# Optimization experiments

Hardware: AMD Instinct MI355X
Metric: run time of the kernel (lower is better)

The kernel has to match this reference:

```python
import jax, jax.numpy as jnp
import numpy as np

N = 20000
E = 320000
IN_C = 256
HID = 64
OUT_C = 64
NUM_LAYERS = 3
HEADS = 8


def setup_inputs() -> dict:
    key = jax.random.key(0)
    ks = jax.random.split(key, 12)
    s_in = 1.0 / np.sqrt(IN_C)
    s_h = 1.0 / np.sqrt(HID)
    inp = {
        "x": jax.random.normal(ks[0], (N, IN_C), dtype=jnp.float32),
        "edge_index": jax.random.randint(ks[1], (2, E), 0, N, dtype=jnp.int64),
        "lin1_w": jax.random.uniform(ks[2], (IN_C, HID), jnp.float32, -s_in, s_in),
        "lin1_b": jnp.zeros((HID,), jnp.float32),
        "wq": jax.random.uniform(ks[3], (NUM_LAYERS, HID, HID), jnp.float32, -s_h, s_h),
        "bq": jnp.zeros((NUM_LAYERS, HID), jnp.float32),
        "wk": jax.random.uniform(ks[4], (NUM_LAYERS, HID, HID), jnp.float32, -s_h, s_h),
        "bk": jnp.zeros((NUM_LAYERS, HID), jnp.float32),
        "wv": jax.random.uniform(ks[5], (NUM_LAYERS, HID, HID), jnp.float32, -s_h, s_h),
        "bv": jnp.zeros((NUM_LAYERS, HID), jnp.float32),
        "lin2_w": jax.random.uniform(ks[6], (HID, OUT_C), jnp.float32, -s_h, s_h),
        "lin2_b": jnp.zeros((OUT_C,), jnp.float32),
    }
    return inp


def reference(x, edge_index, lin1_w, lin1_b, wq, bq, wk, bk, wv, bv, lin2_w, lin2_b):
    n = x.shape[0]
    C = lin1_w.shape[1]
    d = C // HEADS  # per-head dim
    inv_sqrt_d = 1.0 / (d ** 0.5)

    # gcn_norm with self-loops (symmetric normalization, edge weights = 1)
    loop = jnp.arange(n, dtype=edge_index.dtype)
    row = jnp.concatenate([edge_index[0], loop])  # source j
    col = jnp.concatenate([edge_index[1], loop])  # target i
    deg = jax.ops.segment_sum(jnp.ones_like(col, dtype=x.dtype), col, num_segments=n)
    dinv = jnp.where(deg > 0, deg ** -0.5, 0.0)
    norm = dinv[row] * dinv[col]  # [E+N]

    # input projection (dropout inactive in eval mode)
    h = jax.nn.relu(x @ lin1_w + lin1_b)
    x_all = h[:, None, :]  # [N, 1, C] growing history

    for l in range(NUM_LAYERS):
        t = x_all.shape[1]
        # node-level projections (linear commutes with gather)
        q = x_all[:, -1] @ wq[l] + bq[l]                      # [N, C]
        k = jnp.einsum("ntc,cd->ntd", x_all, wk[l]) + bk[l]   # [N, t, C]
        v = jnp.einsum("ntc,cd->ntd", x_all, wv[l]) + bv[l]   # [N, t, C]
        # per-edge multi-head attention of target's latest repr over source history
        Qe = q[col].reshape(-1, HEADS, d)                      # [E', H, d]
        Ke = k[row].reshape(-1, t, HEADS, d)                   # [E', t, H, d]
        Ve = v[row].reshape(-1, t, HEADS, d)
        scores = jnp.einsum("ehd,ethd->eht", Qe, Ke) * inv_sqrt_d
        attn = jax.nn.softmax(scores, axis=-1)                 # [E', H, t]
        msg = jnp.einsum("eht,ethd->ehd", attn, Ve).reshape(-1, C)
        msg = msg * norm[:, None]
        out = jax.ops.segment_sum(msg, col, num_segments=n)    # sum aggregation
        out = jax.nn.relu(out)
        x_all = jnp.concatenate([x_all, out[:, None, :]], axis=1)

    logits = x_all[:, -1] @ lin2_w + lin2_b
    return jax.nn.log_softmax(logits, axis=1)
```

## Files before the change

### kernel.cpp

```cpp
#include <hip/hip_runtime.h>
#include <math.h>

#define HID 64
#define HEADS 8
#define NUM_LAYERS 3

typedef __attribute__((ext_vector_type(8))) short bf16x8;
typedef __attribute__((ext_vector_type(4))) float f32x4;

__device__ __forceinline__ unsigned short f2bf(float f) {
    union { float f; unsigned int u; } cv; cv.f = f;
    unsigned int u = cv.u;
    unsigned int r = (u + 0x7FFFu + ((u >> 16) & 1u)) >> 16;
    return (unsigned short)r;
}
__device__ __forceinline__ float bflo(unsigned int u) {
    union { unsigned int u; float f; } cv; cv.u = u << 16; return cv.f;
}
__device__ __forceinline__ float bfhi(unsigned int u) {
    union { unsigned int u; float f; } cv; cv.u = u & 0xFFFF0000u; return cv.f;
}
__device__ __forceinline__ unsigned relu_pk(unsigned u) {
    unsigned m = ((u & 0x8000u) ? 0u : 0xFFFFu) |
                 ((u & 0x80000000u) ? 0u : 0xFFFF0000u);
    return u & m;
}

__global__ void k_count(const int* __restrict__ col, int* __restrict__ counts, int E) {
    int e = blockIdx.x * blockDim.x + threadIdx.x;
    if (e < E) atomicAdd(&counts[col[e]], 1);
}

__global__ __launch_bounds__(1024) void k_scan(const int* __restrict__ counts,
                                               int* __restrict__ start,
                                               float* __restrict__ dinv, int n) {
    __shared__ int wsum[16];
    int tid = threadIdx.x;
    int lane = tid & 63, wv = tid >> 6;
    int ipt = (n + 1023) >> 10;
    int c0 = tid * ipt;
    int c1 = min(n, c0 + ipt);
    int s = 0;
    for (int i = c0; i < c1; ++i) s += counts[i];
    int x = s;
#pragma unroll
    for (int off = 1; off < 64; off <<= 1) {
        int y = __shfl_up(x, off);
        if (lane >= off) x += y;
    }
    if (lane == 63) wsum[wv] = x;
    __syncthreads();
    if (wv == 0 && lane < 16) {
        int t2 = wsum[lane];
#pragma unroll
        for (int off = 1; off < 16; off <<= 1) {
            int y = __shfl_up(t2, off);
            if (lane >= off) t2 += y;
        }
        wsum[lane] = t2;
    }
    __syncthreads();
    int waveoff = (wv > 0) ? wsum[wv - 1] : 0;
    int run = waveoff + x - s;
    for (int i = c0; i < c1; ++i) {
        int v = counts[i];
        start[i] = run;
        dinv[i] = rsqrtf((float)(v + 1));
        run += v;
    }
    if (tid == 0) start[n] = wsum[15];
}

__global__ void k_scatter(const int* __restrict__ ei, const int* __restrict__ start,
                          int* __restrict__ fill, int* __restrict__ ebuf, int E) {
    int e = blockIdx.x * blockDim.x + threadIdx.x;
    if (e >= E) return;
    int r = ei[e], c = ei[E + e];
    int pos = start[c] + atomicAdd(&fill[c], 1);
    ebuf[pos] = r;
}

#define ALD 72

__device__ __forceinline__ void stage_w_bf16(unsigned short* Wt,
                                             const float* __restrict__ w, int tid) {
    for (int idx = tid; idx < 1024; idx += 256) {
        int k = idx >> 4, n4 = (idx & 15) * 4;
        float4 wv = *(const float4*)&w[k * 64 + n4];
        Wt[(n4 + 0) * ALD + k] = f2bf(wv.x);
        Wt[(n4 + 1) * ALD + k] = f2bf(wv.y);
        Wt[(n4 + 2) * ALD + k] = f2bf(wv.z);
        Wt[(n4 + 3) * ALD + k] = f2bf(wv.w);
    }
}

__device__ __forceinline__ void mfma_step(const unsigned short* Alds,
                                          const unsigned short* Wt,
                                          int tid, f32x4 acc[4]) {
    int lane = tid & 63;
    int m0 = (tid >> 6) * 16;
    int c16 = lane & 15, quad = lane >> 4;
    const unsigned short* ar = &Alds[(m0 + c16) * ALD + quad * 8];
    bf16x8 a0 = *(const bf16x8*)ar;
    bf16x8 a1 = *(const bf16x8*)(ar + 32);
#pragma unroll
    for (int nt = 0; nt < 4; ++nt) {
        const unsigned short* br = &Wt[(nt * 16 + c16) * ALD + quad * 8];
        bf16x8 b0 = *(const bf16x8*)br;
        bf16x8 b1 = *(const bf16x8*)(br + 32);
        acc[nt] = __builtin_amdgcn_mfma_f32_16x16x32_bf16(a0, b0, acc[nt], 0, 0, 0);
        acc[nt] = __builtin_amdgcn_mfma_f32_16x16x32_bf16(a1, b1, acc[nt], 0, 0, 0);
    }
}

__global__ __launch_bounds__(256, 4) void k_lin1(
    const float* __restrict__ x, const float* __restrict__ w,
    const float* __restrict__ b, const float* __restrict__ wv0,
    const float* __restrict__ bv0, unsigned short* __restrict__ h,
    unsigned short* __restrict__ kv, int n) {
    __shared__ __align__(16) unsigned short Alds[64 * ALD];
    __shared__ __align__(16) unsigned short Wt[64 * ALD];
    int tid = threadIdx.x;
    int node0 = blockIdx.x * 64;
    f32x4 acc[4];
#pragma unroll
    for (int nt = 0; nt < 4; ++nt) acc[nt] = (f32x4){0.f, 0.f, 0.f, 0.f};

    for (int kc = 0; kc < 256; kc += 64) {
        __syncthreads();
        stage_w_bf16(Wt, w + kc * 64, tid);
        for (int idx = tid; idx < 1024; idx += 256) {
            int r = idx >> 4, c4 = (idx & 15) * 4;
            int node = node0 + r;
            float4 v = make_float4(0.f, 0.f, 0.f, 0.f);
            if (node < n) v = *(const float4*)&x[(size_t)node * 256 + kc + c4];
            Alds[r * ALD + c4 + 0] = f2bf(v.x);
            Alds[r * ALD + c4 + 1] = f2bf(v.y);
            Alds[r * ALD + c4 + 2] = f2bf(v.z);
            Alds[r * ALD + c4 + 3] = f2bf(v.w);
        }
        __syncthreads();
        mfma_step(Alds, Wt, tid, acc);
    }
    int lane = tid & 63;
    int m0 = (tid >> 6) * 16, c16 = lane & 15, quad = lane >> 4;
    float bias[4];
#pragma unroll
    for (int nt = 0; nt < 4; ++nt) bias[nt] = b[nt * 16 + c16];

    __syncthreads();
    stage_w_bf16(Wt, wv0, tid);
#pragma unroll
    for (int i = 0; i < 4; ++i) {
        int row = m0 + quad * 4 + i;
        int node = node0 + row;
#pragma unroll
        for (int nt = 0; nt < 4; ++nt) {
            unsigned short hb = f2bf(fmaxf(acc[nt][i] + bias[nt], 0.f));
            Alds[row * ALD + nt * 16 + c16] = hb;
            if (node < n) h[(size_t)node * 64 + nt * 16 + c16] = hb;
        }
    }
    __syncthreads();
    f32x4 acc2[4];
#pragma unroll
    for (int nt = 0; nt < 4; ++nt) acc2[nt] = (f32x4){0.f, 0.f, 0.f, 0.f};
    mfma_step(Alds, Wt, tid, acc2);
    float bias2[4];
#pragma unroll
    for (int nt = 0; nt < 4; ++nt) bias2[nt] = bv0[nt * 16 + c16];
#pragma unroll
    for (int i = 0; i < 4; ++i) {
        int node = node0 + m0 + quad * 4 + i;
        if (node < n) {
#pragma unroll
            for (int nt = 0; nt < 4; ++nt)
                kv[(size_t)node * 64 + nt * 16 + c16] = f2bf(acc2[nt][i] + bias2[nt]);
        }
    }
}

__global__ __launch_bounds__(256, 4) void k_qkv(
    const unsigned short* __restrict__ xsbase,
    const float* __restrict__ wq, const float* __restrict__ bq,
    const float* __restrict__ wk, const float* __restrict__ bk,
    const float* __restrict__ wv, const float* __restrict__ bv,
    float* __restrict__ q, unsigned short* __restrict__ kv,
    int n, int layer, int t, int kv_stride) {
    int job = blockIdx.y;
    const unsigned short* src; const float* w; const float* b; bool relu_in;
    int kv_off = 0;
    if (job == 0) {
        src = xsbase + (size_t)layer * n * 64;
        w = wq + layer * 4096; b = bq + layer * 64;
        relu_in = (layer >= 1);
    } else if (job <= t) {
        int s = job - 1;
        src = xsbase + (size_t)s * n * 64;
        w = wk + layer * 4096; b = bk + layer * 64;
        kv_off = s * 128;
        relu_in = (s >= 1);
    } else {
        int s = job - t - 1;
        src = xsbase + (size_t)s * n * 64;
        w = wv + layer * 4096; b = bv + layer * 64;
        kv_off = s * 128 + 64;
        relu_in = (s >= 1);
    }
    __shared__ __align__(16) unsigned short Alds[64 * ALD];
    __shared__ __align__(16) unsigned short Wt[64 * ALD];
    int tid = threadIdx.x;
    int node0 = blockIdx.x * 64;
    stage_w_bf16(Wt, w, tid);
    for (int idx = tid; idx < 512; idx += 256) {
        int r = idx >> 3, seg = idx & 7;
        int node = node0 + r;
        uint4 u = make_uint4(0u, 0u, 0u, 0u);
        if (node < n) u = *(const uint4*)&src[(size_t)node * 64 + seg * 8];
        if (relu_in) {
            u.x = relu_pk(u.x); u.y = relu_pk(u.y);
            u.z = relu_pk(u.z); u.w = relu_pk(u.w);
        }
        *(uint4*)&Alds[r * ALD + seg * 8] = u;
    }
    __syncthreads();
    f32x4 acc[4];
#pragma unroll
    for (int nt = 0; nt < 4; ++nt) acc[nt] = (f32x4){0.f, 0.f, 0.f, 0.f};
    mfma_step(Alds, Wt, tid, acc);

    int lane = tid & 63;
    int m0 = (tid >> 6) * 16, c16 = lane & 15, quad = lane >> 4;
    float bias[4];
#pragma unroll
    for (int nt = 0; nt < 4; ++nt) bias[nt] = b[nt * 16 + c16];
    if (job == 0) {
#pragma unroll
        for (int i = 0; i < 4; ++i) {
            int node = node0 + m0 + quad * 4 + i;
            if (node < n) {
#pragma unroll
                for (int nt = 0; nt < 4; ++nt)
                    q[(size_t)node * 64 + nt * 16 + c16] = acc[nt][i] + bias[nt];
            }
        }
    } else {
#pragma unroll
        for (int i = 0; i < 4; ++i) {
            int node = node0 + m0 + quad * 4 + i;
            if (node < n) {
#pragma unroll
                for (int nt = 0; nt < 4; ++nt)
                    kv[(size_t)node * kv_stride + kv_off + nt * 16 + c16] =
                        f2bf(acc[nt][i] + bias[nt]);
            }
        }
    }
}

template <int T>
__global__ __launch_bounds__(256) void k_attn_g(
    const int* __restrict__ start, const int* __restrict__ ebuf,
    const float* __restrict__ dinv, const float* __restrict__ q,
    const unsigned short* __restrict__ kv, unsigned short* __restrict__ outp, int n) {
    const int KVS = (T == 1) ? 64 : T * 128;
    int node = (int)((blockIdx.x * (size_t)blockDim.x + threadIdx.x) >> 6);
    int lane = threadIdx.x & 63;
    if (node >= n) return;
    int g = lane >> 3;
    int cb = (lane & 7) * 8;
    const float isd = 0.35355339059327373f;

    float qv[8];
    if (T > 1) {
        float4 q0 = *(const float4*)&q[(size_t)node * 64 + cb];
        float4 q1 = *(const float4*)&q[(size_t)node * 64 + cb + 4];
        qv[0] = q0.x; qv[1] = q0.y; qv[2] = q0.z; qv[3] = q0.w;
        qv[4] = q1.x; qv[5] = q1.y; qv[6] = q1.z; qv[7] = q1.w;
    }
    float dc = dinv[node];
    int s0 = start[node];
    int cnt = start[node + 1] - s0 + 1;

    float acc[8];
#pragma unroll
    for (int k = 0; k < 8; ++k) acc[k] = 0.f;

    for (int base = 0; base < cnt; base += 8) {
        int idx = base + g;
        bool valid = idx < cnt;
        int r = node;
        if (valid && idx > 0) r = ebuf[s0 + idx - 1];
        float dr = valid ? dinv[r] : 0.f;
        const unsigned short* rkv = kv + (size_t)r * KVS;

        float sc[T];
        float wgt;
        if (T > 1) {
            float m = -1e30f;
#pragma unroll
            for (int s = 0; s < T; ++s) {
                uint4 ku = *(const uint4*)&rkv[s * 128 + cb];
                float p = qv[0] * bflo(ku.x) + qv[1] * bfhi(ku.x)
                        + qv[2] * bflo(ku.y) + qv[3] * bfhi(ku.y)
                        + qv[4] * bflo(ku.z) + qv[5] * bfhi(ku.z)
                        + qv[6] * bflo(ku.w) + qv[7] * bfhi(ku.w);
                p *= isd;
                sc[s] = p;
                m = fmaxf(m, p);
            }
            float denom = 0.f;
#pragma unroll
            for (int s = 0; s < T; ++s) { sc[s] = __expf(sc[s] - m); denom += sc[s]; }
            wgt = dr / denom;
        } else {
            sc[0] = 1.f;
            wgt = dr;
        }

        float mg[8];
#pragma unroll
        for (int k = 0; k < 8; ++k) mg[k] = 0.f;
#pragma unroll
        for (int s = 0; s < T; ++s) {
            uint4 vu = *(const uint4*)&rkv[((T == 1) ? 0 : s * 128 + 64) + cb];
            float wv_ = sc[s];
            mg[0] += wv_ * bflo(vu.x); mg[1] += wv_ * bfhi(vu.x);
            mg[2] += wv_ * bflo(vu.y); mg[3] += wv_ * bfhi(vu.y);
            mg[4] += wv_ * bflo(vu.z); mg[5] += wv_ * bfhi(vu.z);
            mg[6] += wv_ * bflo(vu.w); mg[7] += wv_ * bfhi(vu.w);
        }
#pragma unroll
        for (int k = 0; k < 8; ++k) acc[k] += wgt * mg[k];
    }

#pragma unroll
    for (int off = 8; off < 64; off <<= 1) {
#pragma unroll
        for (int k = 0; k < 8; ++k) acc[k] += __shfl_xor(acc[k], off);
    }
    if (g == 0) {
        ushort4 o0, o1;
        o0.x = f2bf(acc[0] * dc); o0.y = f2bf(acc[1] * dc);
        o0.z = f2bf(acc[2] * dc); o0.w = f2bf(acc[3] * dc);
        o1.x = f2bf(acc[4] * dc); o1.y = f2bf(acc[5] * dc);
        o1.z = f2bf(acc[6] * dc); o1.w = f2bf(acc[7] * dc);
        *(ushort4*)&outp[(size_t)node * 64 + cb] = o0;
        *(ushort4*)&outp[(size_t)node * 64 + cb + 4] = o1;
    }
}

__global__ __launch_bounds__(256) void k_attn3f(
    const int* __restrict__ start, const int* __restrict__ ebuf,
    const float* __restrict__ dinv, const float* __restrict__ q,
    const unsigned short* __restrict__ kv,
    const float* __restrict__ w2, const float* __restrict__ b2,
    float* __restrict__ outp, int n) {
    const int T = 3, KVS = 384;
    int node = (int)((blockIdx.x * (size_t)blockDim.x + threadIdx.x) >> 6);
    int lane = threadIdx.x & 63;
    if (node >= n) return;
    int g = lane >> 3;
    int cb = (lane & 7) * 8;
    const float isd = 0.35355339059327373f;

    float qv[8];
    {
        float4 q0 = *(const float4*)&q[(size_t)node * 64 + cb];
        float4 q1 = *(const float4*)&q[(size_t)node * 64 + cb + 4];
        qv[0] = q0.x; qv[1] = q0.y; qv[2] = q0.z; qv[3] = q0.w;
        qv[4] = q1.x; qv[5] = q1.y; qv[6] = q1.z; qv[7] = q1.w;
    }
    float dc = dinv[node];
    int s0 = start[node];
    int cnt = start[node + 1] - s0 + 1;

    float acc[8];
#pragma unroll
    for (int k = 0; k < 8; ++k) acc[k] = 0.f;

    for (int base = 0; base < cnt; base += 8) {
        int idx = base + g;
        bool valid = idx < cnt;
        int r = node;
        if (valid && idx > 0) r = ebuf[s0 + idx - 1];
        float dr = valid ? dinv[r] : 0.f;
        const unsigned short* rkv = kv + (size_t)r * KVS;

        float sc[T];
        float m = -1e30f;
#pragma unroll
        for (int s = 0; s < T; ++s) {
            uint4 ku = *(const uint4*)&rkv[s * 128 + cb];
            float p = qv[0] * bflo(ku.x) + qv[1] * bfhi(ku.x)
                    + qv[2] * bflo(ku.y) + qv[3] * bfhi(ku.y)
                    + qv[4] * bflo(ku.z) + qv[5] * bfhi(ku.z)
                    + qv[6] * bflo(ku.w) + qv[7] * bfhi(ku.w);
            p *= isd;
            sc[s] = p;
            m = fmaxf(m, p);
        }
        float denom = 0.f;
#pragma unroll
        for (int s = 0; s < T; ++s) { sc[s] = __expf(sc[s] - m); denom += sc[s]; }
        float wgt = dr / denom;

        float mg[8];
#pragma unroll
        for (int k = 0; k < 8; ++k) mg[k] = 0.f;
#pragma unroll
        for (int s = 0; s < T; ++s) {
            uint4 vu = *(const uint4*)&rkv[s * 128 + 64 + cb];
            float wv_ = sc[s];
            mg[0] += wv_ * bflo(vu.x); mg[1] += wv_ * bfhi(vu.x);
            mg[2] += wv_ * bflo(vu.y); mg[3] += wv_ * bfhi(vu.y);
            mg[4] += wv_ * bflo(vu.z); mg[5] += wv_ * bfhi(vu.z);
            mg[6] += wv_ * bflo(vu.w); mg[7] += wv_ * bfhi(vu.w);
        }
#pragma unroll
        for (int k = 0; k < 8; ++k) acc[k] += wgt * mg[k];
    }

#pragma unroll
    for (int off = 8; off < 64; off <<= 1) {
#pragma unroll
        for (int k = 0; k < 8; ++k) acc[k] += __shfl_xor(acc[k], off);
    }
    float lg = b2[lane];
#pragma unroll
    for (int c = 0; c < 64; ++c) {
        float xc = fmaxf(__shfl(acc[c & 7], c >> 3) * dc, 0.f);
        lg += xc * w2[c * 64 + lane];
    }
    float mx = lg;
#pragma unroll
    for (int off = 1; off < 64; off <<= 1) mx = fmaxf(mx, __shfl_xor(mx, off));
    float e = __expf(lg - mx);
    float ssum = e;
#pragma unroll
    for (int off = 1; off < 64; off <<= 1) ssum += __shfl_xor(ssum, off);
    outp[(size_t)node * 64 + lane] = lg - mx - __logf(ssum);
}

extern "C" void kernel_launch(void* const* d_in, const int* in_sizes, int n_in,
                              void* d_out, int out_size, void* d_ws, size_t ws_size,
                              hipStream_t stream) {
    const float* x  = (const float*)d_in[0];
    const int*   ei = (const int*)d_in[1];
    const float* w1 = (const float*)d_in[2];
    const float* b1 = (const float*)d_in[3];
    const float* wq = (const float*)d_in[4];
    const float* bq = (const float*)d_in[5];
    const float* wk = (const float*)d_in[6];
    const float* bk = (const float*)d_in[7];
    const float* wv = (const float*)d_in[8];
    const float* bv = (const float*)d_in[9];
    const float* w2 = (const float*)d_in[10];
    const float* b2 = (const float*)d_in[11];
    float* outp = (float*)d_out;

    int n = in_sizes[0] / 256;
    int E = in_sizes[1] / 2;

    float* ws = (float*)d_ws;
    size_t off = 0;
    float* dinv = ws + off; off += (size_t)n;
    float* q    = ws + off; off += (size_t)n * 64;
    unsigned short* xsU = (unsigned short*)(ws + off); off += (size_t)n * 96;
    unsigned short* kvU = (unsigned short*)(ws + off); off += (size_t)n * 192;
    int* wsI    = (int*)(ws + off);
    int* counts = wsI;
    int* fill   = wsI + n;
    int* startA = wsI + 2 * n;
    int* ebuf   = wsI + 3 * n + 1;

    hipMemsetAsync(counts, 0, 2 * (size_t)n * sizeof(int), stream);
    k_count<<<(E + 255) / 256, 256, 0, stream>>>(ei + E, counts, E);
    k_scan<<<1, 1024, 0, stream>>>(counts, startA, dinv, n);
    k_scatter<<<(E + 255) / 256, 256, 0, stream>>>(ei, startA, fill, ebuf, E);

    k_lin1<<<(n + 63) / 64, 256, 0, stream>>>(x, w1, b1, wv, bv, xsU, kvU, n);

    int attn_grid = (int)(((size_t)n * 64 + 255) / 256);

    k_attn_g<1><<<attn_grid, 256, 0, stream>>>(startA, ebuf, dinv, q, kvU,
                                               xsU + (size_t)n * 64, n);
    {
        dim3 grid((n + 63) / 64, 5);
        k_qkv<<<grid, 256, 0, stream>>>(xsU, wq, bq, wk, bk, wv, bv,
                                        q, kvU, n, 1, 2, 256);
        k_attn_g<2><<<attn_grid, 256, 0, stream>>>(startA, ebuf, dinv, q, kvU,
                                                   xsU + (size_t)n * 128, n);
    }
    {
        dim3 grid((n + 63) / 64, 7);
        k_qkv<<<grid, 256, 0, stream>>>(xsU, wq, bq, wk, bk, wv, bv,
                                        q, kvU, n, 2, 3, 384);
        k_attn3f<<<attn_grid, 256, 0, stream>>>(startA, ebuf, dinv, q, kvU,
                                                w2, b2, outp, n);
    }
}
```

Measured before the change: 263.5 us.

## Fuse degree count into lin1 launch, bf16 queries, prefetch neighbor indices via shuffles

The edge-degree counting kernel is merged into the lin1 GEMM launch as a second grid row, so both run concurrently and one launch disappears. The scatter pass reuses the counts array by decrementing it, which removes the separate fill buffer and halves the memset. Queries are now stored as bf16 instead of fp32, halving their traffic at some cost in precision. The attention kernels preload up to 64 neighbor indices and their dinv values once per wave and broadcast them with shuffles, replacing repeated per-iteration gathers.

```diff
diff --git a/kernel.cpp b/kernel.cpp
--- a/kernel.cpp
+++ b/kernel.cpp
@@ -26,9 +26,111 @@
     return u & m;
 }
 
-__global__ void k_count(const int* __restrict__ col, int* __restrict__ counts, int E) {
-    int e = blockIdx.x * blockDim.x + threadIdx.x;
-    if (e < E) atomicAdd(&counts[col[e]], 1);
+#define ALD 72
+
+__device__ __forceinline__ void stage_w_bf16(unsigned short* Wt,
+                                             const float* __restrict__ w, int tid) {
+    for (int idx = tid; idx < 1024; idx += 256) {
+        int k = idx >> 4, n4 = (idx & 15) * 4;
+        float4 wv = *(const float4*)&w[k * 64 + n4];
+        Wt[(n4 + 0) * ALD + k] = f2bf(wv.x);
+        Wt[(n4 + 1) * ALD + k] = f2bf(wv.y);
+        Wt[(n4 + 2) * ALD + k] = f2bf(wv.z);
+        Wt[(n4 + 3) * ALD + k] = f2bf(wv.w);
+    }
+}
+
+__device__ __forceinline__ void mfma_step(const unsigned short* Alds,
+                                          const unsigned short* Wt,
+                                          int tid, f32x4 acc[4]) {
+    int lane = tid & 63;
+    int m0 = (tid >> 6) * 16;
+    int c16 = lane & 15, quad = lane >> 4;
+    const unsigned short* ar = &Alds[(m0 + c16) * ALD + quad * 8];
+    bf16x8 a0 = *(const bf16x8*)ar;
+    bf16x8 a1 = *(const bf16x8*)(ar + 32);
+#pragma unroll
+    for (int nt = 0; nt < 4; ++nt) {
+        const unsigned short* br = &Wt[(nt * 16 + c16) * ALD + quad * 8];
+        bf16x8 b0 = *(const bf16x8*)br;
+        bf16x8 b1 = *(const bf16x8*)(br + 32);
+        acc[nt] = __builtin_amdgcn_mfma_f32_16x16x32_bf16(a0, b0, acc[nt], 0, 0, 0);
+        acc[nt] = __builtin_amdgcn_mfma_f32_16x16x32_bf16(a1, b1, acc[nt], 0, 0, 0);
+    }
+}
+
+__global__ __launch_bounds__(256, 4) void k_lin1c(
+    const float* __restrict__ x, const float* __restrict__ w,
+    const float* __restrict__ b, const float* __restrict__ wv0,
+    const float* __restrict__ bv0, unsigned short* __restrict__ h,
+    unsigned short* __restrict__ kv, int n,
+    const int* __restrict__ col, int* __restrict__ counts, int E, int gx) {
+    __shared__ __align__(16) unsigned short Alds[64 * ALD];
+    __shared__ __align__(16) unsigned short Wt[64 * ALD];
+    int tid = threadIdx.x;
+    if (blockIdx.y == 1) {
+        int stride = gx * 256;
+        for (int e = blockIdx.x * 256 + tid; e < E; e += stride)
+            atomicAdd(&counts[col[e]], 1);
+        return;
+    }
+    int node0 = blockIdx.x * 64;
+    f32x4 acc[4];
+#pragma unroll
+    for (int nt = 0; nt < 4; ++nt) acc[nt] = (f32x4){0.f, 0.f, 0.f, 0.f};
+
+    for (int kc = 0; kc < 256; kc += 64) {
+        __syncthreads();
+        stage_w_bf16(Wt, w + kc * 64, tid);
+        for (int idx = tid; idx < 1024; idx += 256) {
+            int r = idx >> 4, c4 = (idx & 15) * 4;
+            int node = node0 + r;
+            float4 v = make_float4(0.f, 0.f, 0.f, 0.f);
+            if (node < n) v = *(const float4*)&x[(size_t)node * 256 + kc + c4];
+            Alds[r * ALD + c4 + 0] = f2bf(v.x);
+            Alds[r * ALD + c4 + 1] = f2bf(v.y);
+            Alds[r * ALD + c4 + 2] = f2bf(v.z);
+            Alds[r * ALD + c4 + 3] = f2bf(v.w);
+        }
+        __syncthreads();
+        mfma_step(Alds, Wt, tid, acc);
+    }
+    int lane = tid & 63;
+    int m0 = (tid >> 6) * 16, c16 = lane & 15, quad = lane >> 4;
+    float bias[4];
+#pragma unroll
+    for (int nt = 0; nt < 4; ++nt) bias[nt] = b[nt * 16 + c16];
+
+    __syncthreads();
+    stage_w_bf16(Wt, wv0, tid);
+#pragma unroll
+    for (int i = 0; i < 4; ++i) {
+        int row = m0 + quad * 4 + i;
+        int node = node0 + row;
+#pragma unroll
+        for (int nt = 0; nt < 4; ++nt) {
+            unsigned short hb = f2bf(fmaxf(acc[nt][i] + bias[nt], 0.f));
+            Alds[row * ALD + nt * 16 + c16] = hb;
+            if (node < n) h[(size_t)node * 64 + nt * 16 + c16] = hb;
+        }
+    }
+    __syncthreads();
+    f32x4 acc2[4];
+#pragma unroll
+    for (int nt = 0; nt < 4; ++nt) acc2[nt] = (f32x4){0.f, 0.f, 0.f, 0.f};
+    mfma_step(Alds, Wt, tid, acc2);
+    float bias2[4];
+#pragma unroll
+    for (int nt = 0; nt < 4; ++nt) bias2[nt] = bv0[nt * 16 + c16];
+#pragma unroll
+    for (int i = 0; i < 4; ++i) {
+        int node = node0 + m0 + quad * 4 + i;
+        if (node < n) {
+#pragma unroll
+            for (int nt = 0; nt < 4; ++nt)
+                kv[(size_t)node * 64 + nt * 16 + c16] = f2bf(acc2[nt][i] + bias2[nt]);
+        }
+    }
 }
 
 __global__ __launch_bounds__(1024) void k_scan(const int* __restrict__ counts,
@@ -72,112 +174,12 @@
 }
 
 __global__ void k_scatter(const int* __restrict__ ei, const int* __restrict__ start,
-                          int* __restrict__ fill, int* __restrict__ ebuf, int E) {
+                          int* __restrict__ counts, int* __restrict__ ebuf, int E) {
     int e = blockIdx.x * blockDim.x + threadIdx.x;
     if (e >= E) return;
     int r = ei[e], c = ei[E + e];
-    int pos = start[c] + atomicAdd(&fill[c], 1);
+    int pos = start[c] + atomicSub(&counts[c], 1) - 1;
     ebuf[pos] = r;
-}
-
-#define ALD 72
-
-__device__ __forceinline__ void stage_w_bf16(unsigned short* Wt,
-                                             const float* __restrict__ w, int tid) {
-    for (int idx = tid; idx < 1024; idx += 256) {
-        int k = idx >> 4, n4 = (idx & 15) * 4;
-        float4 wv = *(const float4*)&w[k * 64 + n4];
-        Wt[(n4 + 0) * ALD + k] = f2bf(wv.x);
-        Wt[(n4 + 1) * ALD + k] = f2bf(wv.y);
-        Wt[(n4 + 2) * ALD + k] = f2bf(wv.z);
-        Wt[(n4 + 3) * ALD + k] = f2bf(wv.w);
-    }
-}
-
-__device__ __forceinline__ void mfma_step(const unsigned short* Alds,
-                                          const unsigned short* Wt,
-                                          int tid, f32x4 acc[4]) {
-    int lane = tid & 63;
-    int m0 = (tid >> 6) * 16;
-    int c16 = lane & 15, quad = lane >> 4;
-    const unsigned short* ar = &Alds[(m0 + c16) * ALD + quad * 8];
-    bf16x8 a0 = *(const bf16x8*)ar;
-    bf16x8 a1 = *(const bf16x8*)(ar + 32);
-#pragma unroll
-    for (int nt = 0; nt < 4; ++nt) {
-        const unsigned short* br = &Wt[(nt * 16 + c16) * ALD + quad * 8];
-        bf16x8 b0 = *(const bf16x8*)br;
-        bf16x8 b1 = *(const bf16x8*)(br + 32);
-        acc[nt] = __builtin_amdgcn_mfma_f32_16x16x32_bf16(a0, b0, acc[nt], 0, 0, 0);
-        acc[nt] = __builtin_amdgcn_mfma_f32_16x16x32_bf16(a1, b1, acc[nt], 0, 0, 0);
-    }
-}
-
-__global__ __launch_bounds__(256, 4) void k_lin1(
-    const float* __restrict__ x, const float* __restrict__ w,
-    const float* __restrict__ b, const float* __restrict__ wv0,
-    const float* __restrict__ bv0, unsigned short* __restrict__ h,
-    unsigned short* __restrict__ kv, int n) {
-    __shared__ __align__(16) unsigned short Alds[64 * ALD];
-    __shared__ __align__(16) unsigned short Wt[64 * ALD];
-    int tid = threadIdx.x;
-    int node0 = blockIdx.x * 64;
-    f32x4 acc[4];
-#pragma unroll
-    for (int nt = 0; nt < 4; ++nt) acc[nt] = (f32x4){0.f, 0.f, 0.f, 0.f};
-
-    for (int kc = 0; kc < 256; kc += 64) {
-        __syncthreads();
-        stage_w_bf16(Wt, w + kc * 64, tid);
-        for (int idx = tid; idx < 1024; idx += 256) {
-            int r = idx >> 4, c4 = (idx & 15) * 4;
-            int node = node0 + r;
-            float4 v = make_float4(0.f, 0.f, 0.f, 0.f);
-            if (node < n) v = *(const float4*)&x[(size_t)node * 256 + kc + c4];
-            Alds[r * ALD + c4 + 0] = f2bf(v.x);
-            Alds[r * ALD + c4 + 1] = f2bf(v.y);
-            Alds[r * ALD + c4 + 2] = f2bf(v.z);
-            Alds[r * ALD + c4 + 3] = f2bf(v.w);
-        }
-        __syncthreads();
-        mfma_step(Alds, Wt, tid, acc);
-    }
-    int lane = tid & 63;
-    int m0 = (tid >> 6) * 16, c16 = lane & 15, quad = lane >> 4;
-    float bias[4];
-#pragma unroll
-    for (int nt = 0; nt < 4; ++nt) bias[nt] = b[nt * 16 + c16];
-
-    __syncthreads();
-    stage_w_bf16(Wt, wv0, tid);
-#pragma unroll
-    for (int i = 0; i < 4; ++i) {
-        int row = m0 + quad * 4 + i;
-        int node = node0 + row;
-#pragma unroll
-        for (int nt = 0; nt < 4; ++nt) {
-            unsigned short hb = f2bf(fmaxf(acc[nt][i] + bias[nt], 0.f));
-            Alds[row * ALD + nt * 16 + c16] = hb;
-            if (node < n) h[(size_t)node * 64 + nt * 16 + c16] = hb;
-        }
-    }
-    __syncthreads();
-    f32x4 acc2[4];
-#pragma unroll
-    for (int nt = 0; nt < 4; ++nt) acc2[nt] = (f32x4){0.f, 0.f, 0.f, 0.f};
-    mfma_step(Alds, Wt, tid, acc2);
-    float bias2[4];
-#pragma unroll
-    for (int nt = 0; nt < 4; ++nt) bias2[nt] = bv0[nt * 16 + c16];
-#pragma unroll
-    for (int i = 0; i < 4; ++i) {
-        int node = node0 + m0 + quad * 4 + i;
-        if (node < n) {
-#pragma unroll
-            for (int nt = 0; nt < 4; ++nt)
-                kv[(size_t)node * 64 + nt * 16 + c16] = f2bf(acc2[nt][i] + bias2[nt]);
-        }
-    }
 }
 
 __global__ __launch_bounds__(256, 4) void k_qkv(
@@ -185,27 +187,28 @@
     const float* __restrict__ wq, const float* __restrict__ bq,
     const float* __restrict__ wk, const float* __restrict__ bk,
     const float* __restrict__ wv, const float* __restrict__ bv,
-    float* __restrict__ q, unsigned short* __restrict__ kv,
+    unsigned short* __restrict__ q, unsigned short* __restrict__ kv,
     int n, int layer, int t, int kv_stride) {
     int job = blockIdx.y;
     const unsigned short* src; const float* w; const float* b; bool relu_in;
-    int kv_off = 0;
+    unsigned short* dst; size_t dstride; int dst_off;
     if (job == 0) {
         src = xsbase + (size_t)layer * n * 64;
         w = wq + layer * 4096; b = bq + layer * 64;
         relu_in = (layer >= 1);
+        dst = q; dstride = 64; dst_off = 0;
     } else if (job <= t) {
         int s = job - 1;
         src = xsbase + (size_t)s * n * 64;
         w = wk + layer * 4096; b = bk + layer * 64;
-        kv_off = s * 128;
         relu_in = (s >= 1);
+        dst = kv; dstride = kv_stride; dst_off = s * 128;
     } else {
         int s = job - t - 1;
         src = xsbase + (size_t)s * n * 64;
         w = wv + layer * 4096; b = bv + layer * 64;
-        kv_off = s * 128 + 64;
         relu_in = (s >= 1);
+        dst = kv; dstride = kv_stride; dst_off = s * 128 + 64;
     }
     __shared__ __align__(16) unsigned short Alds[64 * ALD];
     __shared__ __align__(16) unsigned short Wt[64 * ALD];
@@ -234,26 +237,14 @@
     float bias[4];
 #pragma unroll
     for (int nt = 0; nt < 4; ++nt) bias[nt] = b[nt * 16 + c16];
-    if (job == 0) {
-#pragma unroll
-        for (int i = 0; i < 4; ++i) {
-            int node = node0 + m0 + quad * 4 + i;
-            if (node < n) {
-#pragma unroll
-                for (int nt = 0; nt < 4; ++nt)
-                    q[(size_t)node * 64 + nt * 16 + c16] = acc[nt][i] + bias[nt];
-            }
-        }
-    } else {
-#pragma unroll
-        for (int i = 0; i < 4; ++i) {
-            int node = node0 + m0 + quad * 4 + i;
-            if (node < n) {
-#pragma unroll
-                for (int nt = 0; nt < 4; ++nt)
-                    kv[(size_t)node * kv_stride + kv_off + nt * 16 + c16] =
-                        f2bf(acc[nt][i] + bias[nt]);
-            }
+#pragma unroll
+    for (int i = 0; i < 4; ++i) {
+        int node = node0 + m0 + quad * 4 + i;
+        if (node < n) {
+#pragma unroll
+            for (int nt = 0; nt < 4; ++nt)
+                dst[(size_t)node * dstride + dst_off + nt * 16 + c16] =
+                    f2bf(acc[nt][i] + bias[nt]);
         }
     }
 }
@@ -261,7 +252,7 @@
 template <int T>
 __global__ __launch_bounds__(256) void k_attn_g(
     const int* __restrict__ start, const int* __restrict__ ebuf,
-    const float* __restrict__ dinv, const float* __restrict__ q,
+    const float* __restrict__ dinv, const unsigned short* __restrict__ qb,
     const unsigned short* __restrict__ kv, unsigned short* __restrict__ outp, int n) {
     const int KVS = (T == 1) ? 64 : T * 128;
     int node = (int)((blockIdx.x * (size_t)blockDim.x + threadIdx.x) >> 6);
@@ -273,15 +264,20 @@
 
     float qv[8];
     if (T > 1) {
-        float4 q0 = *(const float4*)&q[(size_t)node * 64 + cb];
-        float4 q1 = *(const float4*)&q[(size_t)node * 64 + cb + 4];
-        qv[0] = q0.x; qv[1] = q0.y; qv[2] = q0.z; qv[3] = q0.w;
-        qv[4] = q1.x; qv[5] = q1.y; qv[6] = q1.z; qv[7] = q1.w;
+        uint4 qu = *(const uint4*)&qb[(size_t)node * 64 + cb];
+        qv[0] = bflo(qu.x); qv[1] = bfhi(qu.x);
+        qv[2] = bflo(qu.y); qv[3] = bfhi(qu.y);
+        qv[4] = bflo(qu.z); qv[5] = bfhi(qu.z);
+        qv[6] = bflo(qu.w); qv[7] = bfhi(qu.w);
     }
     float dc = dinv[node];
     int s0 = start[node];
     int cnt = start[node + 1] - s0 + 1;
 
+    int rp = node;
+    if (lane >= 1 && lane < cnt) rp = ebuf[s0 + lane - 1];
+    float dp = dinv[rp];
+
     float acc[8];
 #pragma unroll
     for (int k = 0; k < 8; ++k) acc[k] = 0.f;
@@ -289,9 +285,10 @@
     for (int base = 0; base < cnt; base += 8) {
         int idx = base + g;
         bool valid = idx < cnt;
-        int r = node;
-        if (valid && idx > 0) r = ebuf[s0 + idx - 1];
-        float dr = valid ? dinv[r] : 0.f;
+        int r = __shfl(rp, idx & 63);
+        float dr = __shfl(dp, idx & 63);
+        if (idx >= 64 && valid) { r = ebuf[s0 + idx - 1]; dr = dinv[r]; }
+        if (!valid) dr = 0.f;
         const unsigned short* rkv = kv + (size_t)r * KVS;
 
         float sc[T];
@@ -352,7 +349,7 @@
 
 __global__ __launch_bounds__(256) void k_attn3f(
     const int* __restrict__ start, const int* __restrict__ ebuf,
-    const float* __restrict__ dinv, const float* __restrict__ q,
+    const float* __restrict__ dinv, const unsigned short* __restrict__ qb,
     const unsigned short* __restrict__ kv,
     const float* __restrict__ w2, const float* __restrict__ b2,
     float* __restrict__ outp, int n) {
@@ -366,15 +363,20 @@
 
     float qv[8];
     {
-        float4 q0 = *(const float4*)&q[(size_t)node * 64 + cb];
-        float4 q1 = *(const float4*)&q[(size_t)node * 64 + cb + 4];
-        qv[0] = q0.x; qv[1] = q0.y; qv[2] = q0.z; qv[3] = q0.w;
-        qv[4] = q1.x; qv[5] = q1.y; qv[6] = q1.z; qv[7] = q1.w;
+        uint4 qu = *(const uint4*)&qb[(size_t)node * 64 + cb];
+        qv[0] = bflo(qu.x); qv[1] = bfhi(qu.x);
+        qv[2] = bflo(qu.y); qv[3] = bfhi(qu.y);
+        qv[4] = bflo(qu.z); qv[5] = bfhi(qu.z);
+        qv[6] = bflo(qu.w); qv[7] = bfhi(qu.w);
     }
     float dc = dinv[node];
     int s0 = start[node];
     int cnt = start[node + 1] - s0 + 1;
 
+    int rp = node;
+    if (lane >= 1 && lane < cnt) rp = ebuf[s0 + lane - 1];
+    float dp = dinv[rp];
+
     float acc[8];
 #pragma unroll
     for (int k = 0; k < 8; ++k) acc[k] = 0.f;
@@ -382,9 +384,10 @@
     for (int base = 0; base < cnt; base += 8) {
         int idx = base + g;
         bool valid = idx < cnt;
-        int r = node;
-        if (valid && idx > 0) r = ebuf[s0 + idx - 1];
-        float dr = valid ? dinv[r] : 0.f;
+        int r = __shfl(rp, idx & 63);
+        float dr = __shfl(dp, idx & 63);
+        if (idx >= 64 && valid) { r = ebuf[s0 + idx - 1]; dr = dinv[r]; }
+        if (!valid) dr = 0.f;
         const unsigned short* rkv = kv + (size_t)r * KVS;
 
         float sc[T];
@@ -465,38 +468,41 @@
     float* ws = (float*)d_ws;
     size_t off = 0;
     float* dinv = ws + off; off += (size_t)n;
-    float* q    = ws + off; off += (size_t)n * 64;
+    unsigned short* qb  = (unsigned short*)(ws + off); off += (size_t)n * 32;
     unsigned short* xsU = (unsigned short*)(ws + off); off += (size_t)n * 96;
     unsigned short* kvU = (unsigned short*)(ws + off); off += (size_t)n * 192;
     int* wsI    = (int*)(ws + off);
     int* counts = wsI;
-    int* fill   = wsI + n;
-    int* startA = wsI + 2 * n;
-    int* ebuf   = wsI + 3 * n + 1;
-
-    hipMemsetAsync(counts, 0, 2 * (size_t)n * sizeof(int), stream);
-    k_count<<<(E + 255) / 256, 256, 0, stream>>>(ei + E, counts, E);
+    int* startA = wsI + n;
+    int* ebuf   = wsI + 2 * n + 1;
+
+    int gx = (n + 63) / 64;
+
+    hipMemsetAsync(counts, 0, (size_t)n * sizeof(int), stream);
+    {
+        dim3 grid(gx, 2);
+        k_lin1c<<<grid, 256, 0, stream>>>(x, w1, b1, wv, bv, xsU, kvU, n,
+                                          ei + E, counts, E, gx);
+    }
     k_scan<<<1, 1024, 0, stream>>>(counts, startA, dinv, n);
-    k_scatter<<<(E + 255) / 256, 256, 0, stream>>>(ei, startA, fill, ebuf, E);
-
-    k_lin1<<<(n + 63) / 64, 256, 0, stream>>>(x, w1, b1, wv, bv, xsU, kvU, n);
+    k_scatter<<<(E + 255) / 256, 256, 0, stream>>>(ei, startA, counts, ebuf, E);
 
     int attn_grid = (int)(((size_t)n * 64 + 255) / 256);
 
-    k_attn_g<1><<<attn_grid, 256, 0, stream>>>(startA, ebuf, dinv, q, kvU,
+    k_attn_g<1><<<attn_grid, 256, 0, stream>>>(startA, ebuf, dinv, qb, kvU,
                                                xsU + (size_t)n * 64, n);
     {
-        dim3 grid((n + 63) / 64, 5);
+        dim3 grid(gx, 5);
         k_qkv<<<grid, 256, 0, stream>>>(xsU, wq, bq, wk, bk, wv, bv,
-                                        q, kvU, n, 1, 2, 256);
-        k_attn_g<2><<<attn_grid, 256, 0, stream>>>(startA, ebuf, dinv, q, kvU,
+                                        qb, kvU, n, 1, 2, 256);
+        k_attn_g<2><<<attn_grid, 256, 0, stream>>>(startA, ebuf, dinv, qb, kvU,
                                                    xsU + (size_t)n * 128, n);
     }
     {
-        dim3 grid((n + 63) / 64, 7);
+        dim3 grid(gx, 7);
         k_qkv<<<grid, 256, 0, stream>>>(xsU, wq, bq, wk, bk, wv, bv,
-                                        q, kvU, n, 2, 3, 384);
-        k_attn3f<<<attn_grid, 256, 0, stream>>>(startA, ebuf, dinv, q, kvU,
+                                        qb, kvU, n, 2, 3, 384);
+        k_attn3f<<<attn_grid, 256, 0, stream>>>(startA, ebuf, dinv, qb, kvU,
                                                 w2, b2, outp, n);
     }
 }
```

After: 265.6 us. About the same (+0.8%).
